# Kernel optimization log

Measured on AMD Instinct MI355X. Metric: run time of the kernel, lower is better.

Reference implementation:

```python
import jax, jax.numpy as jnp
import numpy as np

B, M, S, E, LC, V, HOPS = 16, 2048, 6, 128, 512, 32000, 3
PAD = 1


def setup_inputs() -> dict:
    key = jax.random.key(0)
    ks = jax.random.split(key, 16)
    story = jax.random.randint(ks[0], (B, M, S), 0, V)
    kb_len = jax.random.randint(ks[1], (B,), 0, M - LC)
    conv_len = jax.random.randint(ks[2], (B,), 0, LC)
    hidden = jax.random.normal(ks[3], (1, B, 2 * E), jnp.float32)
    dh_outputs = jax.random.normal(ks[4], (B, LC, E), jnp.float32)
    tf_hidden = jax.random.normal(ks[5], (B, E), jnp.float32)
    query_vector = jax.random.normal(ks[6], (B, E), jnp.float32)
    global_pointer = jax.random.uniform(ks[7], (B, M), jnp.float32)
    C = jax.random.normal(ks[8], (HOPS + 1, V, E), jnp.float32) * 0.1
    C = C.at[:, PAD, :].set(0.0)  # padding_idx row is zero
    s = 0.05
    wA1 = jax.random.normal(ks[9], (2 * E, E), jnp.float32) * s
    bA1 = jnp.zeros((E,), jnp.float32)
    wA2 = jax.random.normal(ks[10], (E, E), jnp.float32) * s
    bA2 = jnp.zeros((E,), jnp.float32)
    wC1 = jax.random.normal(ks[11], (2 * E, E), jnp.float32) * s
    bC1 = jnp.zeros((E,), jnp.float32)
    wC2 = jax.random.normal(ks[12], (E, E), jnp.float32) * s
    bC2 = jnp.zeros((E,), jnp.float32)
    wf = jax.random.normal(ks[13], (2 * E, E), jnp.float32) * s
    bf = jnp.zeros((E,), jnp.float32)
    return dict(story=story, kb_len=kb_len, conv_len=conv_len, hidden=hidden,
                dh_outputs=dh_outputs, tf_hidden=tf_hidden, query_vector=query_vector,
                global_pointer=global_pointer, C=C, wA1=wA1, bA1=bA1, wA2=wA2, bA2=bA2,
                wC1=wC1, bC1=bC1, wC2=wC2, bC2=bC2, wf=wf, bf=bf)


def _lrelu(x):
    return jnp.where(x > 0, x, 0.1 * x)  # LeakyReLU(0.1)


def _mlp(x, w1, b1, w2, b2):
    return _lrelu(x @ w1 + b1) @ w2 + b2


def _add_lm(mem, kb_len, conv_len, dh):
    # mem: [B,M,E]; add dh[bi,:conv_len[bi]] into rows [kb_len, kb_len+conv_len)
    pos = jnp.arange(mem.shape[1])[None, :]            # [1,M]
    idx = pos - kb_len[:, None]                        # [B,M]
    mask = (idx >= 0) & (idx < conv_len[:, None])
    gathered = jnp.take_along_axis(dh, jnp.clip(idx, 0, dh.shape[1] - 1)[..., None], axis=1)
    return mem + jnp.where(mask[..., None], gathered, 0.0)


def reference(story, kb_len, conv_len, hidden, dh_outputs, tf_hidden,
              query_vector, global_pointer, C, wA1, bA1, wA2, bA2,
              wC1, bC1, wC2, bC2, wf, bf):
    # --- load_ent_memory: build m_story_ent (dropout off / eval mode) ---
    u = _lrelu(hidden[0] @ wf + bf)                    # hidden.squeeze(0) -> [B,E]
    tf = jnp.broadcast_to(tf_hidden[:, None, :], (B, M, E))
    m_story = []
    eC = None
    for hop in range(HOPS):
        eA = _add_lm(C[hop][story].sum(2), kb_len, conv_len, dh_outputs)       # [B,M,E]
        eA = _mlp(jnp.concatenate([eA, tf], -1), wA1, bA1, wA2, bA2)
        logit = jnp.einsum('bme,be->bm', eA, u)
        p = jax.nn.softmax(logit, axis=1)
        eC = _add_lm(C[hop + 1][story].sum(2), kb_len, conv_len, dh_outputs)   # [B,M,E]
        eC = _mlp(jnp.concatenate([eC, tf], -1), wC1, bC1, wC2, bC2)
        u = u + jnp.einsum('bme,bm->be', eC, p)
        m_story.append(eA)
    m_story.append(eC)
    # --- forward(query_vector, global_pointer) ---
    uq = query_vector
    gp = global_pointer[..., None]                     # [B,M,1]
    prob_logits = None
    prob_soft = None
    for hop in range(HOPS):
        mA = m_story[hop] * gp
        prob_logits = jnp.einsum('bme,be->bm', mA, uq)
        prob_soft = jax.nn.softmax(prob_logits, axis=1)
        mC = m_story[hop + 1] * gp
        uq = uq + jnp.einsum('bme,bm->be', mC, prob_soft)
    return (prob_soft, prob_logits)
```

## Files before the change

kernel.cpp:

```cpp
#include <hip/hip_runtime.h>
#include <math.h>

#define BB 16
#define MM 2048
#define SS 6
#define EE 128
#define LCC 512
#define VV 32000

typedef __attribute__((ext_vector_type(8))) __bf16 bf16x8;
typedef __attribute__((ext_vector_type(4))) float f32x4;

#define HS_STRIDE 136

static __device__ inline unsigned short bfbits(float x) {
    __bf16 h = (__bf16)x;
    return __builtin_bit_cast(unsigned short, h);
}

#define N_W1  (128 * 128)
#define N_W2  (128 * 128)
#define N_UQ  (BB * EE)
#define N_SMALL (N_W1 + N_W2 + 2 * N_UQ)
#define SMALL_BLOCKS 144
#define TFB_BLOCKS 8
#define N_C   (3 * VV * EE)
#define C_BLOCKS 6000
#define PREP_BLOCKS (SMALL_BLOCKS + TFB_BLOCKS + C_BLOCKS)

__global__ __launch_bounds__(256)
void prep_kernel(const float* __restrict__ W1, const float* __restrict__ W2,
                 const float* __restrict__ C,
                 const float* __restrict__ tf, const float* __restrict__ b1,
                 __bf16* __restrict__ w1t, __bf16* __restrict__ w2t,
                 float* __restrict__ tfb1, __bf16* __restrict__ Cb,
                 float* __restrict__ uqA, float* __restrict__ uqB)
{
    if (blockIdx.x < SMALL_BLOCKS) {
        int i = blockIdx.x * 256 + threadIdx.x;
        if (i < N_W1) { const int n = i >> 7, k = i & 127; w1t[i] = (__bf16)W1[k * EE + n]; return; }
        i -= N_W1;
        if (i < N_W2) { const int n = i >> 7, k = i & 127; w2t[i] = (__bf16)W2[k * EE + n]; return; }
        i -= N_W2;
        if (i < N_UQ) { uqA[i] = 0.f; return; }
        i -= N_UQ;
        if (i < N_UQ) { uqB[i] = 0.f; }
        return;
    }
    if (blockIdx.x < SMALL_BLOCKS + TFB_BLOCKS) {
        const int i = (blockIdx.x - SMALL_BLOCKS) * 256 + threadIdx.x;
        const int b = i >> 7, n = i & 127;
        float s = b1[n];
        #pragma unroll 4
        for (int k = 0; k < 128; ++k)
            s += tf[b * EE + k] * W1[(128 + k) * EE + n];
        tfb1[i] = s;
        return;
    }
    const size_t base = ((size_t)(blockIdx.x - SMALL_BLOCKS - TFB_BLOCKS) * 256 + threadIdx.x) * 8;
    const float4 a = *(const float4*)&C[base];
    const float4 b = *(const float4*)&C[base + 4];
    bf16x8 h;
    h[0] = (__bf16)a.x; h[1] = (__bf16)a.y; h[2] = (__bf16)a.z; h[3] = (__bf16)a.w;
    h[4] = (__bf16)b.x; h[5] = (__bf16)b.y; h[6] = (__bf16)b.z; h[7] = (__bf16)b.w;
    *(bf16x8*)&Cb[base] = h;
}

__global__ __launch_bounds__(256)
void embed_mlp_mfma(const int* __restrict__ story,
                    const int* __restrict__ kb_len,
                    const int* __restrict__ conv_len,
                    const float* __restrict__ dh,
                    const __bf16* __restrict__ Cb,
                    const __bf16* __restrict__ w1t, const float* __restrict__ tfb1,
                    const __bf16* __restrict__ w2t, const float* __restrict__ b2,
                    const float* __restrict__ gp, const float* __restrict__ query,
                    __bf16* __restrict__ mout, float* __restrict__ lbuf0)
{
    __shared__ __bf16 Xs[32 * HS_STRIDE];
    __shared__ int    sidx[32 * SS];
    __bf16* Hs   = Xs;
    float*  plog = (float*)Xs;

    const int bid  = blockIdx.x;
    const int hop  = bid >> 10;
    const int row0 = (bid & 1023) * 32;
    const int b    = row0 >> 11;
    const int tid  = threadIdx.x;

    const __bf16* Ck = Cb + (size_t)hop * VV * EE;

    for (int i = tid; i < 32 * SS; i += 256) sidx[i] = story[(size_t)row0 * SS + i];

    const int kb   = kb_len[b];
    const int cl   = conv_len[b];
    const int rgrp = tid >> 4;
    const int e8   = (tid & 15) * 8;
    __syncthreads();

    for (int chunk = 0; chunk < 2; ++chunk) {
        const int r  = chunk * 16 + rgrp;
        const int* si = &sidx[r * SS];
        bf16x8 v[SS];
        #pragma unroll
        for (int s = 0; s < SS; ++s)
            v[s] = *(const bf16x8*)&Ck[(size_t)si[s] * EE + e8];
        const int j = ((row0 + r) & (MM - 1)) - kb;
        float4 a0 = {0.f, 0.f, 0.f, 0.f};
        float4 a1 = {0.f, 0.f, 0.f, 0.f};
        if (j >= 0 && j < cl) {
            a0 = *(const float4*)&dh[((size_t)b * LCC + j) * EE + e8];
            a1 = *(const float4*)&dh[((size_t)b * LCC + j) * EE + e8 + 4];
        }
        #pragma unroll
        for (int s = 0; s < SS; ++s) {
            a0.x += (float)v[s][0]; a0.y += (float)v[s][1];
            a0.z += (float)v[s][2]; a0.w += (float)v[s][3];
            a1.x += (float)v[s][4]; a1.y += (float)v[s][5];
            a1.z += (float)v[s][6]; a1.w += (float)v[s][7];
        }
        bf16x8 pk;
        pk[0] = (__bf16)a0.x; pk[1] = (__bf16)a0.y;
        pk[2] = (__bf16)a0.z; pk[3] = (__bf16)a0.w;
        pk[4] = (__bf16)a1.x; pk[5] = (__bf16)a1.y;
        pk[6] = (__bf16)a1.z; pk[7] = (__bf16)a1.w;
        *(bf16x8*)&Xs[r * HS_STRIDE + e8] = pk;
    }
    __syncthreads();

    const int w       = tid >> 6;
    const int lane    = tid & 63;
    const int lr      = lane & 15;
    const int lk      = lane >> 4;
    const int colbase = w * 32;

    f32x4 acc1[2][2];
    #pragma unroll
    for (int i = 0; i < 2; ++i)
        #pragma unroll
        for (int j = 0; j < 2; ++j) acc1[i][j] = (f32x4){0.f, 0.f, 0.f, 0.f};

    for (int ks = 0; ks < 4; ++ks) {
        bf16x8 a[2], bw[2];
        #pragma unroll
        for (int mt = 0; mt < 2; ++mt)
            a[mt] = *(const bf16x8*)&Xs[(mt * 16 + lr) * HS_STRIDE + ks * 32 + lk * 8];
        #pragma unroll
        for (int nt = 0; nt < 2; ++nt)
            bw[nt] = *(const bf16x8*)&w1t[(size_t)(colbase + nt * 16 + lr) * 128 + ks * 32 + lk * 8];
        #pragma unroll
        for (int mt = 0; mt < 2; ++mt)
            #pragma unroll
            for (int nt = 0; nt < 2; ++nt)
                acc1[mt][nt] = __builtin_amdgcn_mfma_f32_16x16x32_bf16(a[mt], bw[nt], acc1[mt][nt], 0, 0, 0);
    }
    __syncthreads();
    {
        const float b1v[2] = { tfb1[b * EE + colbase + lr], tfb1[b * EE + colbase + 16 + lr] };
        #pragma unroll
        for (int mt = 0; mt < 2; ++mt)
            #pragma unroll
            for (int nt = 0; nt < 2; ++nt)
                #pragma unroll
                for (int reg = 0; reg < 4; ++reg) {
                    float h = acc1[mt][nt][reg] + b1v[nt];
                    h = (h > 0.f) ? h : 0.1f * h;
                    Hs[(mt * 16 + lk * 4 + reg) * HS_STRIDE + colbase + nt * 16 + lr] = (__bf16)h;
                }
    }
    __syncthreads();

    f32x4 acc2[2][2];
    #pragma unroll
    for (int i = 0; i < 2; ++i)
        #pragma unroll
        for (int j = 0; j < 2; ++j) acc2[i][j] = (f32x4){0.f, 0.f, 0.f, 0.f};

    for (int ks = 0; ks < 4; ++ks) {
        bf16x8 a[2], bw[2];
        #pragma unroll
        for (int mt = 0; mt < 2; ++mt)
            a[mt] = *(const bf16x8*)&Hs[(mt * 16 + lr) * HS_STRIDE + ks * 32 + lk * 8];
        #pragma unroll
        for (int nt = 0; nt < 2; ++nt)
            bw[nt] = *(const bf16x8*)&w2t[(size_t)(colbase + nt * 16 + lr) * 128 + ks * 32 + lk * 8];
        #pragma unroll
        for (int mt = 0; mt < 2; ++mt)
            #pragma unroll
            for (int nt = 0; nt < 2; ++nt)
                acc2[mt][nt] = __builtin_amdgcn_mfma_f32_16x16x32_bf16(a[mt], bw[nt], acc2[mt][nt], 0, 0, 0);
    }

    const float b2v[2] = { b2[colbase + lr], b2[colbase + 16 + lr] };

    if (hop == 0) {
        const float qv0 = query[b * EE + colbase + lr];
        const float qv1 = query[b * EE + colbase + 16 + lr];
        __syncthreads();
        #pragma unroll
        for (int mt = 0; mt < 2; ++mt)
            #pragma unroll
            for (int reg = 0; reg < 4; ++reg) {
                float p = (acc2[mt][0][reg] + b2v[0]) * qv0
                        + (acc2[mt][1][reg] + b2v[1]) * qv1;
                p += __shfl_xor(p, 1, 64);
                p += __shfl_xor(p, 2, 64);
                p += __shfl_xor(p, 4, 64);
                p += __shfl_xor(p, 8, 64);
                if (lr == 0) plog[(mt * 16 + lk * 4 + reg) * 4 + w] = p;
            }
        __syncthreads();
        if (tid < 32) {
            const float l = plog[tid * 4] + plog[tid * 4 + 1] + plog[tid * 4 + 2] + plog[tid * 4 + 3];
            lbuf0[row0 + tid] = l * gp[row0 + tid];
        }
    } else {
        __bf16* out = mout + (size_t)(hop - 1) * 32768 * EE;
        #pragma unroll
        for (int mt = 0; mt < 2; ++mt)
            #pragma unroll
            for (int nt = 0; nt < 2; ++nt)
                #pragma unroll
                for (int reg = 0; reg < 4; ++reg) {
                    const int rg_ = row0 + mt * 16 + lk * 4 + reg;
                    out[(size_t)rg_ * EE + colbase + nt * 16 + lr] =
                        (__bf16)(acc2[mt][nt][reg] + b2v[nt]);
                }
    }
}

__global__ __launch_bounds__(256)
void update_kernel(const __bf16* __restrict__ mk, const float* __restrict__ gp,
                   const float* __restrict__ lbuf, float* __restrict__ uq)
{
    __shared__ float redm[4], reds[4];
    __shared__ float wls[64];
    __shared__ float part[4][128];

    const int b      = blockIdx.x >> 5;
    const int rloc0  = (blockIdx.x & 31) * 64;
    const int tid    = threadIdx.x;
    const int lane   = tid & 63;
    const int w      = tid >> 6;
    const float* lb  = lbuf + (size_t)b * MM;

    float v[8];
    float mx = -1e30f;
    #pragma unroll
    for (int i = 0; i < 8; ++i) { v[i] = lb[i * 256 + tid]; mx = fmaxf(mx, v[i]); }
    #pragma unroll
    for (int off = 32; off > 0; off >>= 1) mx = fmaxf(mx, __shfl_xor(mx, off, 64));
    if (lane == 0) redm[w] = mx;
    __syncthreads();
    mx = fmaxf(fmaxf(redm[0], redm[1]), fmaxf(redm[2], redm[3]));
    float sum = 0.f;
    #pragma unroll
    for (int i = 0; i < 8; ++i) sum += __expf(v[i] - mx);
    #pragma unroll
    for (int off = 32; off > 0; off >>= 1) sum += __shfl_xor(sum, off, 64);
    if (lane == 0) reds[w] = sum;
    __syncthreads();
    const float inv = 1.f / (reds[0] + reds[1] + reds[2] + reds[3]);

    if (tid < 64)
        wls[tid] = gp[(size_t)b * MM + rloc0 + tid] * __expf(lb[rloc0 + tid] - mx) * inv;
    __syncthreads();

    const int rgrp = tid >> 4;
    const int e8   = (tid & 15) * 8;
    float acc[8];
    #pragma unroll
    for (int q = 0; q < 8; ++q) acc[q] = 0.f;
    #pragma unroll
    for (int p = 0; p < 4; ++p) {
        const int rl  = p * 16 + rgrp;
        const float wg = wls[rl];
        const bf16x8 vv = *(const bf16x8*)&mk[((size_t)b * MM + rloc0 + rl) * EE + e8];
        #pragma unroll
        for (int q = 0; q < 8; ++q) acc[q] += wg * (float)vv[q];
    }
    #pragma unroll
    for (int q = 0; q < 8; ++q) {
        acc[q] += __shfl_xor(acc[q], 16, 64);
        acc[q] += __shfl_xor(acc[q], 32, 64);
    }
    if (lane < 16) {
        #pragma unroll
        for (int q = 0; q < 8; ++q) part[w][e8 + q] = acc[q];
    }
    __syncthreads();
    if (tid < 128) {
        const float s = part[0][tid] + part[1][tid] + part[2][tid] + part[3][tid];
        atomicAdd(&uq[b * EE + tid], s);
    }
}

__global__ __launch_bounds__(256)
void logits_kernel(const __bf16* __restrict__ mk, const float* __restrict__ gp,
                   const float* __restrict__ query, const float* __restrict__ uqa,
                   const float* __restrict__ uqb, float* __restrict__ out)
{
    __shared__ float uqs[128];
    const int row0 = blockIdx.x * 64;
    const int b    = row0 >> 11;
    const int tid  = threadIdx.x;
    if (tid < 128)
        uqs[tid] = query[b * EE + tid] + uqa[b * EE + tid]
                 + (uqb ? uqb[b * EE + tid] : 0.f);
    __syncthreads();
    const int w = tid >> 6, lane = tid & 63;
    const int g = lane >> 4, l16 = lane & 15;
    float u[8];
    #pragma unroll
    for (int j = 0; j < 8; ++j) u[j] = uqs[l16 * 8 + j];
    #pragma unroll
    for (int it = 0; it < 4; ++it) {
        const int row = row0 + it * 16 + w * 4 + g;
        const bf16x8 v = *(const bf16x8*)&mk[(size_t)row * EE + l16 * 8];
        float p = 0.f;
        #pragma unroll
        for (int j = 0; j < 8; ++j) p += (float)v[j] * u[j];
        p += __shfl_xor(p, 1, 64);
        p += __shfl_xor(p, 2, 64);
        p += __shfl_xor(p, 4, 64);
        p += __shfl_xor(p, 8, 64);
        if (l16 == 0) out[row] = p * gp[row];
    }
}

__global__ __launch_bounds__(256)
void softmax_final(const float* __restrict__ logits, float* __restrict__ soft)
{
    __shared__ float redm[4], reds[4];
    const int b = blockIdx.x, tid = threadIdx.x;
    const int lane = tid & 63, w = tid >> 6;
    const float* lb = logits + (size_t)b * MM;
    float v[8];
    float mx = -1e30f;
    #pragma unroll
    for (int i = 0; i < 8; ++i) { v[i] = lb[i * 256 + tid]; mx = fmaxf(mx, v[i]); }
    #pragma unroll
    for (int off = 32; off > 0; off >>= 1) mx = fmaxf(mx, __shfl_xor(mx, off, 64));
    if (lane == 0) redm[w] = mx;
    __syncthreads();
    mx = fmaxf(fmaxf(redm[0], redm[1]), fmaxf(redm[2], redm[3]));
    float sum = 0.f;
    #pragma unroll
    for (int i = 0; i < 8; ++i) { v[i] = __expf(v[i] - mx); sum += v[i]; }
    #pragma unroll
    for (int off = 32; off > 0; off >>= 1) sum += __shfl_xor(sum, off, 64);
    if (lane == 0) reds[w] = sum;
    __syncthreads();
    const float inv = 1.f / (reds[0] + reds[1] + reds[2] + reds[3]);
    #pragma unroll
    for (int i = 0; i < 8; ++i) soft[(size_t)b * MM + i * 256 + tid] = v[i] * inv;
}

extern "C" void kernel_launch(void* const* d_in, const int* in_sizes, int n_in,
                              void* d_out, int out_size, void* d_ws, size_t ws_size,
                              hipStream_t stream) {
    const int*   story    = (const int*)d_in[0];
    const int*   kb_len   = (const int*)d_in[1];
    const int*   conv_len = (const int*)d_in[2];
    const float* dh       = (const float*)d_in[4];
    const float* tf       = (const float*)d_in[5];
    const float* query    = (const float*)d_in[6];
    const float* gp       = (const float*)d_in[7];
    const float* C        = (const float*)d_in[8];
    const float* wA1      = (const float*)d_in[9];
    const float* bA1      = (const float*)d_in[10];
    const float* wA2      = (const float*)d_in[11];
    const float* bA2      = (const float*)d_in[12];

    char* ws = (char*)d_ws;
    const size_t M_ELEMS = (size_t)32768 * EE;
    size_t off = 0;
    __bf16* m    = (__bf16*)(ws + off); off += 2 * M_ELEMS * sizeof(__bf16);
    __bf16* Cb   = (__bf16*)(ws + off); off += (size_t)N_C * sizeof(__bf16);
    __bf16* w1t  = (__bf16*)(ws + off); off += 128 * 128 * sizeof(__bf16);
    __bf16* w2t  = (__bf16*)(ws + off); off += 128 * 128 * sizeof(__bf16);
    float*  tfb1 = (float*)(ws + off);  off += (size_t)BB * EE * sizeof(float);
    float*  lbuf = (float*)(ws + off);  off += (size_t)BB * MM * sizeof(float);
    float*  uqA  = (float*)(ws + off);  off += (size_t)BB * EE * sizeof(float);
    float*  uqB  = (float*)(ws + off);  off += (size_t)BB * EE * sizeof(float);

    float* out_soft   = (float*)d_out;
    float* out_logits = out_soft + (size_t)BB * MM;

    prep_kernel<<<PREP_BLOCKS, 256, 0, stream>>>(wA1, wA2, C, tf, bA1,
                                                 w1t, w2t, tfb1, Cb, uqA, uqB);
    embed_mlp_mfma<<<3072, 256, 0, stream>>>(story, kb_len, conv_len, dh, Cb,
                                             w1t, tfb1, w2t, bA2, gp, query, m, lbuf);
    update_kernel<<<512, 256, 0, stream>>>(m, gp, lbuf, uqA);
    logits_kernel<<<512, 256, 0, stream>>>(m, gp, query, uqA, nullptr, lbuf);
    update_kernel<<<512, 256, 0, stream>>>(m + M_ELEMS, gp, lbuf, uqB);
    logits_kernel<<<512, 256, 0, stream>>>(m + M_ELEMS, gp, query, uqA, uqB, out_logits);
    softmax_final<<<BB, 256, 0, stream>>>(out_logits, out_soft);
}
```

Baseline: 192.8 us.

## Fold first MLP layer into embedding table and dh before gather

Uses linearity of the first MLP layer: C rows and dh rows are multiplied by W1 once, as a precomputed GEMM, and the per-row embedding sum then gathers already-projected vectors, adds the tf bias, and applies LeakyReLU directly. This removes the first MFMA GEMM and one LDS round-trip from the per-row embed kernel. In exchange a dense 96000x128x128 GEMM over the vocabulary table is added, plus a 8192-row one over dh, where before there was only a bf16 conversion. Precision also shifts, because C is rounded to bf16 before the projection and the projected values are rounded to bf16 again.

```diff
diff --git a/kernel.cpp b/kernel.cpp
--- a/kernel.cpp
+++ b/kernel.cpp
@@ -13,28 +13,20 @@
 
 #define HS_STRIDE 136
 
-static __device__ inline unsigned short bfbits(float x) {
-    __bf16 h = (__bf16)x;
-    return __builtin_bit_cast(unsigned short, h);
-}
-
 #define N_W1  (128 * 128)
 #define N_W2  (128 * 128)
 #define N_UQ  (BB * EE)
 #define N_SMALL (N_W1 + N_W2 + 2 * N_UQ)
 #define SMALL_BLOCKS 144
 #define TFB_BLOCKS 8
-#define N_C   (3 * VV * EE)
-#define C_BLOCKS 6000
-#define PREP_BLOCKS (SMALL_BLOCKS + TFB_BLOCKS + C_BLOCKS)
-
-__global__ __launch_bounds__(256)
-void prep_kernel(const float* __restrict__ W1, const float* __restrict__ W2,
-                 const float* __restrict__ C,
-                 const float* __restrict__ tf, const float* __restrict__ b1,
-                 __bf16* __restrict__ w1t, __bf16* __restrict__ w2t,
-                 float* __restrict__ tfb1, __bf16* __restrict__ Cb,
-                 float* __restrict__ uqA, float* __restrict__ uqB)
+#define PA_BLOCKS (SMALL_BLOCKS + TFB_BLOCKS)
+
+__global__ __launch_bounds__(256)
+void prep_a(const float* __restrict__ W1, const float* __restrict__ W2,
+            const float* __restrict__ tf, const float* __restrict__ b1,
+            __bf16* __restrict__ w1t, __bf16* __restrict__ w2t,
+            float* __restrict__ tfb1,
+            float* __restrict__ uqA, float* __restrict__ uqB)
 {
     if (blockIdx.x < SMALL_BLOCKS) {
         int i = blockIdx.x * 256 + threadIdx.x;
@@ -47,40 +39,121 @@
         if (i < N_UQ) { uqB[i] = 0.f; }
         return;
     }
-    if (blockIdx.x < SMALL_BLOCKS + TFB_BLOCKS) {
-        const int i = (blockIdx.x - SMALL_BLOCKS) * 256 + threadIdx.x;
-        const int b = i >> 7, n = i & 127;
-        float s = b1[n];
-        #pragma unroll 4
-        for (int k = 0; k < 128; ++k)
-            s += tf[b * EE + k] * W1[(128 + k) * EE + n];
-        tfb1[i] = s;
-        return;
-    }
-    const size_t base = ((size_t)(blockIdx.x - SMALL_BLOCKS - TFB_BLOCKS) * 256 + threadIdx.x) * 8;
-    const float4 a = *(const float4*)&C[base];
-    const float4 b = *(const float4*)&C[base + 4];
-    bf16x8 h;
-    h[0] = (__bf16)a.x; h[1] = (__bf16)a.y; h[2] = (__bf16)a.z; h[3] = (__bf16)a.w;
-    h[4] = (__bf16)b.x; h[5] = (__bf16)b.y; h[6] = (__bf16)b.z; h[7] = (__bf16)b.w;
-    *(bf16x8*)&Cb[base] = h;
+    const int i = (blockIdx.x - SMALL_BLOCKS) * 256 + threadIdx.x;
+    const int b = i >> 7, n = i & 127;
+    float s = b1[n];
+    #pragma unroll 4
+    for (int k = 0; k < 128; ++k)
+        s += tf[b * EE + k] * W1[(128 + k) * EE + n];
+    tfb1[i] = s;
+}
+
+#define PB_C   3000
+#define PB_DH  256
+#define PB_BLOCKS (PB_C + PB_DH)
+
+__global__ __launch_bounds__(256)
+void prep_gemm(const float* __restrict__ C, const float* __restrict__ dh,
+               const __bf16* __restrict__ w1t,
+               __bf16* __restrict__ Cp, float* __restrict__ dhp)
+{
+    __shared__ __bf16 Xs[32 * HS_STRIDE];
+
+    const int bid  = blockIdx.x;
+    const int tid  = threadIdx.x;
+    const bool isC = bid < PB_C;
+    const int rgrp = tid >> 4;
+    const int e8   = (tid & 15) * 8;
+
+    size_t row0g;
+    const float* src;
+    if (isC) {
+        const int hop  = bid / 1000;
+        const int vr0  = (bid % 1000) * 32;
+        row0g = (size_t)hop * VV + vr0;
+        src   = C + row0g * EE;
+    } else {
+        row0g = (size_t)(bid - PB_C) * 32;
+        src   = dh + row0g * EE;
+    }
+
+    for (int chunk = 0; chunk < 2; ++chunk) {
+        const int r = chunk * 16 + rgrp;
+        const float4 a0 = *(const float4*)&src[(size_t)r * EE + e8];
+        const float4 a1 = *(const float4*)&src[(size_t)r * EE + e8 + 4];
+        bf16x8 pk;
+        pk[0] = (__bf16)a0.x; pk[1] = (__bf16)a0.y;
+        pk[2] = (__bf16)a0.z; pk[3] = (__bf16)a0.w;
+        pk[4] = (__bf16)a1.x; pk[5] = (__bf16)a1.y;
+        pk[6] = (__bf16)a1.z; pk[7] = (__bf16)a1.w;
+        *(bf16x8*)&Xs[r * HS_STRIDE + e8] = pk;
+    }
+    __syncthreads();
+
+    const int w       = tid >> 6;
+    const int lane    = tid & 63;
+    const int lr      = lane & 15;
+    const int lk      = lane >> 4;
+    const int colbase = w * 32;
+
+    f32x4 acc[2][2];
+    #pragma unroll
+    for (int i = 0; i < 2; ++i)
+        #pragma unroll
+        for (int j = 0; j < 2; ++j) acc[i][j] = (f32x4){0.f, 0.f, 0.f, 0.f};
+
+    for (int ks = 0; ks < 4; ++ks) {
+        bf16x8 a[2], bw[2];
+        #pragma unroll
+        for (int mt = 0; mt < 2; ++mt)
+            a[mt] = *(const bf16x8*)&Xs[(mt * 16 + lr) * HS_STRIDE + ks * 32 + lk * 8];
+        #pragma unroll
+        for (int nt = 0; nt < 2; ++nt)
+            bw[nt] = *(const bf16x8*)&w1t[(size_t)(colbase + nt * 16 + lr) * 128 + ks * 32 + lk * 8];
+        #pragma unroll
+        for (int mt = 0; mt < 2; ++mt)
+            #pragma unroll
+            for (int nt = 0; nt < 2; ++nt)
+                acc[mt][nt] = __builtin_amdgcn_mfma_f32_16x16x32_bf16(a[mt], bw[nt], acc[mt][nt], 0, 0, 0);
+    }
+
+    if (isC) {
+        __bf16* out = Cp + row0g * EE;
+        #pragma unroll
+        for (int mt = 0; mt < 2; ++mt)
+            #pragma unroll
+            for (int nt = 0; nt < 2; ++nt)
+                #pragma unroll
+                for (int reg = 0; reg < 4; ++reg)
+                    out[(size_t)(mt * 16 + lk * 4 + reg) * EE + colbase + nt * 16 + lr] =
+                        (__bf16)acc[mt][nt][reg];
+    } else {
+        float* out = dhp + row0g * EE;
+        #pragma unroll
+        for (int mt = 0; mt < 2; ++mt)
+            #pragma unroll
+            for (int nt = 0; nt < 2; ++nt)
+                #pragma unroll
+                for (int reg = 0; reg < 4; ++reg)
+                    out[(size_t)(mt * 16 + lk * 4 + reg) * EE + colbase + nt * 16 + lr] =
+                        acc[mt][nt][reg];
+    }
 }
 
 __global__ __launch_bounds__(256)
 void embed_mlp_mfma(const int* __restrict__ story,
                     const int* __restrict__ kb_len,
                     const int* __restrict__ conv_len,
-                    const float* __restrict__ dh,
-                    const __bf16* __restrict__ Cb,
-                    const __bf16* __restrict__ w1t, const float* __restrict__ tfb1,
+                    const float* __restrict__ dhp,
+                    const __bf16* __restrict__ Cp,
+                    const float* __restrict__ tfb1,
                     const __bf16* __restrict__ w2t, const float* __restrict__ b2,
                     const float* __restrict__ gp, const float* __restrict__ query,
                     __bf16* __restrict__ mout, float* __restrict__ lbuf0)
 {
-    __shared__ __bf16 Xs[32 * HS_STRIDE];
+    __shared__ __bf16 Hs[32 * HS_STRIDE];
     __shared__ int    sidx[32 * SS];
-    __bf16* Hs   = Xs;
-    float*  plog = (float*)Xs;
+    float* plog = (float*)Hs;
 
     const int bid  = blockIdx.x;
     const int hop  = bid >> 10;
@@ -88,7 +161,7 @@
     const int b    = row0 >> 11;
     const int tid  = threadIdx.x;
 
-    const __bf16* Ck = Cb + (size_t)hop * VV * EE;
+    const __bf16* Ck = Cp + (size_t)hop * VV * EE;
 
     for (int i = tid; i < 32 * SS; i += 256) sidx[i] = story[(size_t)row0 * SS + i];
 
@@ -96,6 +169,8 @@
     const int cl   = conv_len[b];
     const int rgrp = tid >> 4;
     const int e8   = (tid & 15) * 8;
+    const float4 t0 = *(const float4*)&tfb1[b * EE + e8];
+    const float4 t1 = *(const float4*)&tfb1[b * EE + e8 + 4];
     __syncthreads();
 
     for (int chunk = 0; chunk < 2; ++chunk) {
@@ -106,11 +181,12 @@
         for (int s = 0; s < SS; ++s)
             v[s] = *(const bf16x8*)&Ck[(size_t)si[s] * EE + e8];
         const int j = ((row0 + r) & (MM - 1)) - kb;
-        float4 a0 = {0.f, 0.f, 0.f, 0.f};
-        float4 a1 = {0.f, 0.f, 0.f, 0.f};
+        float4 a0 = t0, a1 = t1;
         if (j >= 0 && j < cl) {
-            a0 = *(const float4*)&dh[((size_t)b * LCC + j) * EE + e8];
-            a1 = *(const float4*)&dh[((size_t)b * LCC + j) * EE + e8 + 4];
+            const float4 d0 = *(const float4*)&dhp[((size_t)b * LCC + j) * EE + e8];
+            const float4 d1 = *(const float4*)&dhp[((size_t)b * LCC + j) * EE + e8 + 4];
+            a0.x += d0.x; a0.y += d0.y; a0.z += d0.z; a0.w += d0.w;
+            a1.x += d1.x; a1.y += d1.y; a1.z += d1.z; a1.w += d1.w;
         }
         #pragma unroll
         for (int s = 0; s < SS; ++s) {
@@ -119,12 +195,14 @@
             a1.x += (float)v[s][4]; a1.y += (float)v[s][5];
             a1.z += (float)v[s][6]; a1.w += (float)v[s][7];
         }
+        float h[8] = {a0.x, a0.y, a0.z, a0.w, a1.x, a1.y, a1.z, a1.w};
         bf16x8 pk;
-        pk[0] = (__bf16)a0.x; pk[1] = (__bf16)a0.y;
-        pk[2] = (__bf16)a0.z; pk[3] = (__bf16)a0.w;
-        pk[4] = (__bf16)a1.x; pk[5] = (__bf16)a1.y;
-        pk[6] = (__bf16)a1.z; pk[7] = (__bf16)a1.w;
-        *(bf16x8*)&Xs[r * HS_STRIDE + e8] = pk;
+        #pragma unroll
+        for (int q = 0; q < 8; ++q) {
+            const float hv = (h[q] > 0.f) ? h[q] : 0.1f * h[q];
+            pk[q] = (__bf16)hv;
+        }
+        *(bf16x8*)&Hs[r * HS_STRIDE + e8] = pk;
     }
     __syncthreads();
 
@@ -133,42 +211,6 @@
     const int lr      = lane & 15;
     const int lk      = lane >> 4;
     const int colbase = w * 32;
-
-    f32x4 acc1[2][2];
-    #pragma unroll
-    for (int i = 0; i < 2; ++i)
-        #pragma unroll
-        for (int j = 0; j < 2; ++j) acc1[i][j] = (f32x4){0.f, 0.f, 0.f, 0.f};
-
-    for (int ks = 0; ks < 4; ++ks) {
-        bf16x8 a[2], bw[2];
-        #pragma unroll
-        for (int mt = 0; mt < 2; ++mt)
-            a[mt] = *(const bf16x8*)&Xs[(mt * 16 + lr) * HS_STRIDE + ks * 32 + lk * 8];
-        #pragma unroll
-        for (int nt = 0; nt < 2; ++nt)
-            bw[nt] = *(const bf16x8*)&w1t[(size_t)(colbase + nt * 16 + lr) * 128 + ks * 32 + lk * 8];
-        #pragma unroll
-        for (int mt = 0; mt < 2; ++mt)
-            #pragma unroll
-            for (int nt = 0; nt < 2; ++nt)
-                acc1[mt][nt] = __builtin_amdgcn_mfma_f32_16x16x32_bf16(a[mt], bw[nt], acc1[mt][nt], 0, 0, 0);
-    }
-    __syncthreads();
-    {
-        const float b1v[2] = { tfb1[b * EE + colbase + lr], tfb1[b * EE + colbase + 16 + lr] };
-        #pragma unroll
-        for (int mt = 0; mt < 2; ++mt)
-            #pragma unroll
-            for (int nt = 0; nt < 2; ++nt)
-                #pragma unroll
-                for (int reg = 0; reg < 4; ++reg) {
-                    float h = acc1[mt][nt][reg] + b1v[nt];
-                    h = (h > 0.f) ? h : 0.1f * h;
-                    Hs[(mt * 16 + lk * 4 + reg) * HS_STRIDE + colbase + nt * 16 + lr] = (__bf16)h;
-                }
-    }
-    __syncthreads();
 
     f32x4 acc2[2][2];
     #pragma unroll
@@ -374,9 +416,11 @@
 
     char* ws = (char*)d_ws;
     const size_t M_ELEMS = (size_t)32768 * EE;
+    const size_t N_C = (size_t)3 * VV * EE;
     size_t off = 0;
     __bf16* m    = (__bf16*)(ws + off); off += 2 * M_ELEMS * sizeof(__bf16);
-    __bf16* Cb   = (__bf16*)(ws + off); off += (size_t)N_C * sizeof(__bf16);
+    __bf16* Cp   = (__bf16*)(ws + off); off += N_C * sizeof(__bf16);
+    float*  dhp  = (float*)(ws + off);  off += (size_t)BB * LCC * EE * sizeof(float);
     __bf16* w1t  = (__bf16*)(ws + off); off += 128 * 128 * sizeof(__bf16);
     __bf16* w2t  = (__bf16*)(ws + off); off += 128 * 128 * sizeof(__bf16);
     float*  tfb1 = (float*)(ws + off);  off += (size_t)BB * EE * sizeof(float);
@@ -387,10 +431,10 @@
     float* out_soft   = (float*)d_out;
     float* out_logits = out_soft + (size_t)BB * MM;
 
-    prep_kernel<<<PREP_BLOCKS, 256, 0, stream>>>(wA1, wA2, C, tf, bA1,
-                                                 w1t, w2t, tfb1, Cb, uqA, uqB);
-    embed_mlp_mfma<<<3072, 256, 0, stream>>>(story, kb_len, conv_len, dh, Cb,
-                                             w1t, tfb1, w2t, bA2, gp, query, m, lbuf);
+    prep_a<<<PA_BLOCKS, 256, 0, stream>>>(wA1, wA2, tf, bA1, w1t, w2t, tfb1, uqA, uqB);
+    prep_gemm<<<PB_BLOCKS, 256, 0, stream>>>(C, dh, w1t, Cp, dhp);
+    embed_mlp_mfma<<<3072, 256, 0, stream>>>(story, kb_len, conv_len, dhp, Cp,
+                                             tfb1, w2t, bA2, gp, query, m, lbuf);
     update_kernel<<<512, 256, 0, stream>>>(m, gp, lbuf, uqA);
     logits_kernel<<<512, 256, 0, stream>>>(m, gp, query, uqA, nullptr, lbuf);
     update_kernel<<<512, 256, 0, stream>>>(m + M_ELEMS, gp, lbuf, uqB);
```

Result: slower. 198.1 us (+2.8%).
